# Kernel tuning notes

Hardware: AMD Instinct MI355X
Metric: run time of the kernel (lower is better)

Reference implementation:

```python
import jax, jax.numpy as jnp
import numpy as np

ATTR_LEN = [2, 4, 4, 2, 6]
CUM = np.concatenate(([0], np.cumsum(ATTR_LEN)))  # [0,2,6,10,12,18]
B, S, D, V = 4096, 200, 64, 100000


def setup_inputs() -> dict:
    key = jax.random.key(0)
    ks = jax.random.split(key, 10)
    x = jax.random.randint(ks[0], (B, S), 0, V)
    # one-hot labels per attribute, concatenated -> [B, 18]
    y_parts = []
    for i, al in enumerate(ATTR_LEN):
        lab = jax.random.randint(jax.random.fold_in(ks[1], i), (B,), 0, al)
        y_parts.append(jax.nn.one_hot(lab, al, dtype=jnp.float32))
    y = jnp.concatenate(y_parts, axis=1)
    emb_table = jax.random.normal(ks[2], (V, D), jnp.float32) * 0.02
    emb_table = emb_table.at[0].set(0.0)  # padding_idx=0
    att_w = jax.random.normal(ks[3], (5, D), jnp.float32) * 0.1
    att_b = jax.random.normal(ks[4], (5,), jnp.float32) * 0.1
    W0 = jax.random.normal(ks[5], (ATTR_LEN[0], D), jnp.float32) * 0.1
    W1 = jax.random.normal(ks[6], (ATTR_LEN[1], D), jnp.float32) * 0.1
    W2 = jax.random.normal(ks[7], (ATTR_LEN[2], D), jnp.float32) * 0.1
    W3 = jax.random.normal(ks[8], (ATTR_LEN[3], D), jnp.float32) * 0.1
    W4 = jax.random.normal(ks[9], (ATTR_LEN[4], D), jnp.float32) * 0.1
    return {"x": x, "y": y, "emb_table": emb_table, "att_w": att_w,
            "att_b": att_b, "W0": W0, "W1": W1, "W2": W2, "W3": W3, "W4": W4}


def reference(x, y, emb_table, att_w, att_b, W0, W1, W2, W3, W4):
    embed = emb_table[x]  # [B, S, D] gather (padding row is zero)
    # 5 per-attribute additive tanh-attention heads, batched over k.
    # Softmax over seq axis is independent per head, so stacking is exact.
    att_u = jnp.tanh(jnp.einsum('bsd,kd->bsk', embed, att_w) + att_b)  # [B,S,5]
    score = jax.nn.softmax(att_u, axis=1)                              # [B,S,5]
    user_rep = jnp.einsum('bsd,bsk->bkd', embed, score)                # [B,5,D]
    Ws = [W0, W1, W2, W3, W4]
    # per-task bias-free linear heads, concatenated -> [B, 18]
    W_user = jnp.concatenate([user_rep[:, i] @ Ws[i].T for i in range(5)], axis=1)
    logits = []
    loss = jnp.float32(0.0)
    for i in range(5):
        Wc = W_user[:, CUM[i]:CUM[i + 1]]
        yc = y[:, CUM[i]:CUM[i + 1]]
        # partial_training=False -> ob = ones -> all rows kept;
        # obj = exp(sum(W*y)) / sum_j exp(W_j)  ==  softmax picked at label
        logp = jax.nn.log_softmax(Wc, axis=1)
        loss = loss + (-jnp.sum(logp * yc) / Wc.shape[0])
        logits.append(jax.nn.softmax(Wc, axis=1))
    logit = jnp.concatenate(logits, axis=1)  # [B, 18]
    return logit, loss
```

## Files before the change

kernel.cpp:

```cpp
#include <hip/hip_runtime.h>
#include <math.h>

#define Bsz 4096
#define Ssz 200
#define Dsz 64
#define NK  5
#define NT  512
#define ROWH 72

typedef _Float16 half_t;
typedef _Float16 h2 __attribute__((ext_vector_type(2)));

__device__ inline h2 shfl_xor_h2(h2 v, int m) {
    int iv = __builtin_bit_cast(int, v);
    iv = __shfl_xor(iv, m);
    return __builtin_bit_cast(h2, iv);
}

__device__ inline float fdot2(h2 a, h2 b, float c) {
#if __has_builtin(__builtin_amdgcn_fdot2)
    return __builtin_amdgcn_fdot2(a, b, c, false);
#else
    return c + (float)a.x * (float)b.x + (float)a.y * (float)b.y;
#endif
}

__global__ void loss_reduce_kernel(const float* __restrict__ pb,
                                   float* __restrict__ loss) {
    const int l = threadIdx.x;
    float s = 0.f;
    for (int i = l; i < Bsz; i += 64) s += pb[i];
#pragma unroll
    for (int m = 32; m >= 1; m >>= 1) s += __shfl_xor(s, m);
    if (l == 0) *loss = s * (1.0f / Bsz);
}

__global__ __launch_bounds__(NT, 8) void tan_kernel(
    const int* __restrict__ x, const float* __restrict__ y,
    const float* __restrict__ emb_table,
    const float* __restrict__ att_w, const float* __restrict__ att_b,
    const float* __restrict__ W0, const float* __restrict__ W1,
    const float* __restrict__ W2, const float* __restrict__ W3,
    const float* __restrict__ W4,
    float* __restrict__ out_logit, float* __restrict__ loss_ws)
{
    __shared__ alignas(16) half_t embh[Ssz * ROWH];
    __shared__ alignas(16) float  att[NK][Ssz];
    __shared__ alignas(16) h2     awh[NK * 32];
    __shared__ alignas(16) half_t urph[8][NK][Dsz];
    __shared__ alignas(16) float  ur[NK][Dsz];
    __shared__ alignas(16) int    xs[Ssz];
    __shared__ float wu[18];

    const int b   = blockIdx.x;
    const int tid = threadIdx.x;
    const int w   = tid >> 6;
    const int l   = tid & 63;

    if (tid < Ssz) xs[tid] = x[b * Ssz + tid];
    if (tid >= 256 && tid < 256 + NK * 32) {
        const int t = tid - 256;
        awh[t] = (h2){(half_t)att_w[2 * t], (half_t)att_w[2 * t + 1]};
    }
    __syncthreads();

    {
        float4 v[7];
#pragma unroll
        for (int p = 0; p < 7; ++p) {
            int i = tid + NT * p;
            if (i > Ssz * 16 - 1) i = Ssz * 16 - 1;
            const int s = i >> 4, c = i & 15;
            v[p] = ((const float4*)(emb_table + (size_t)xs[s] * Dsz))[c];
        }
#pragma unroll
        for (int p = 0; p < 7; ++p) {
            const int i = tid + NT * p;
            if (p < 6 || i < Ssz * 16) {
                const int s = i >> 4, c = i & 15;
                h2 a  = (h2){(half_t)v[p].x, (half_t)v[p].y};
                h2 b2 = (h2){(half_t)v[p].z, (half_t)v[p].w};
                uint2 u = { __builtin_bit_cast(unsigned, a),
                            __builtin_bit_cast(unsigned, b2) };
                *(uint2*)(embh + s * ROWH + c * 4) = u;
            }
        }
    }
    __syncthreads();

    if (tid < 2 * Ssz) {
        const int s = tid >> 1, h = tid & 1;
        union { uint4 q[4]; h2 hh[16]; } ue;
        const uint4* rp = (const uint4*)(embh + s * ROWH + h * 32);
#pragma unroll
        for (int i = 0; i < 4; ++i) ue.q[i] = rp[i];
        float acc[NK];
#pragma unroll 1
        for (int k = 0; k < NK; ++k) {
            union { uint4 q[4]; h2 hh[16]; } ua;
            const uint4* ap = (const uint4*)(awh + k * 32 + h * 16);
#pragma unroll
            for (int i = 0; i < 4; ++i) ua.q[i] = ap[i];
            float a = 0.f;
#pragma unroll
            for (int i = 0; i < 16; ++i) a = fdot2(ue.hh[i], ua.hh[i], a);
            acc[k] = a;
        }
#pragma unroll
        for (int k = 0; k < NK; ++k) acc[k] += __shfl_xor(acc[k], 1);
        if (h == 0) {
#pragma unroll
            for (int k = 0; k < NK; ++k) att[k][s] = tanhf(acc[k] + att_b[k]);
        }
    }
    __syncthreads();

    if (w < NK) {
        const int k = w;
        float vals[4];
        float mx = -1e30f;
#pragma unroll
        for (int j = 0; j < 4; ++j) {
            int s = l + 64 * j;
            vals[j] = (s < Ssz) ? att[k][s] : -1e30f;
            mx = fmaxf(mx, vals[j]);
        }
#pragma unroll
        for (int m = 32; m >= 1; m >>= 1) mx = fmaxf(mx, __shfl_xor(mx, m));
        float sum = 0.f;
#pragma unroll
        for (int j = 0; j < 4; ++j) {
            vals[j] = __expf(vals[j] - mx);
            sum += vals[j];
        }
#pragma unroll
        for (int m = 32; m >= 1; m >>= 1) sum += __shfl_xor(sum, m);
        float inv = 1.0f / sum;
#pragma unroll
        for (int j = 0; j < 4; ++j) {
            int s = l + 64 * j;
            if (s < Ssz) att[k][s] = vals[j] * inv;
        }
    }
    __syncthreads();

    {
        const int c = tid & 7;
        const int j = tid >> 3;
        h2 acc[NK][4];
#pragma unroll
        for (int k = 0; k < NK; ++k)
#pragma unroll
            for (int i = 0; i < 4; ++i) acc[k][i] = (h2){(half_t)0, (half_t)0};
#pragma unroll
        for (int t = 0; t < 4; ++t) {
            const int s = j + 64 * t;
            if (s < Ssz) {
                union { uint4 q; h2 hh[4]; } u;
                u.q = *(const uint4*)(embh + s * ROWH + c * 8);
#pragma unroll
                for (int k = 0; k < NK; ++k) {
                    half_t f = (half_t)att[k][s];
                    h2 sc = (h2){f, f};
#pragma unroll
                    for (int i = 0; i < 4; ++i) acc[k][i] += u.hh[i] * sc;
                }
            }
        }
#pragma unroll
        for (int k = 0; k < NK; ++k)
#pragma unroll
            for (int i = 0; i < 4; ++i) {
                acc[k][i] += shfl_xor_h2(acc[k][i], 8);
                acc[k][i] += shfl_xor_h2(acc[k][i], 16);
                acc[k][i] += shfl_xor_h2(acc[k][i], 32);
            }
        if (l < 8) {
#pragma unroll
            for (int k = 0; k < NK; ++k) {
                union { h2 a[4]; uint4 q; } uu;
#pragma unroll
                for (int i = 0; i < 4; ++i) uu.a[i] = acc[k][i];
                *(uint4*)(&urph[w][k][l * 8]) = uu.q;
            }
        }
    }
    __syncthreads();

    if (tid < NK * Dsz) {
        const int k = tid >> 6, d = tid & 63;
        float ssum = 0.f;
#pragma unroll
        for (int jj = 0; jj < 8; ++jj) ssum += (float)urph[jj][k][d];
        ur[k][d] = ssum;
    }
    __syncthreads();

    for (int j = w; j < 18; j += 8) {
        const float* Wp; int g, c0;
        if      (j < 2)  { g = 0; c0 = 0;  Wp = W0; }
        else if (j < 6)  { g = 1; c0 = 2;  Wp = W1; }
        else if (j < 10) { g = 2; c0 = 6;  Wp = W2; }
        else if (j < 12) { g = 3; c0 = 10; Wp = W3; }
        else             { g = 4; c0 = 12; Wp = W4; }
        float p = ur[g][l] * Wp[(j - c0) * Dsz + l];
#pragma unroll
        for (int m = 32; m >= 1; m >>= 1) p += __shfl_xor(p, m);
        if (l == 0) wu[j] = p;
    }
    __syncthreads();

    if (w == 0) {
        float lossb = 0.f;
        if (l < NK) {
            const int LEN[5] = {2, 4, 4, 2, 6};
            const int C0[5]  = {0, 2, 6, 10, 12};
            const int g = l, c0 = C0[g], len = LEN[g];
            float* op = out_logit + (size_t)b * 18;
            const float* yp = y + (size_t)b * 18;
            float mx = -1e30f;
            for (int j = 0; j < len; ++j) mx = fmaxf(mx, wu[c0 + j]);
            float sum = 0.f;
            for (int j = 0; j < len; ++j) sum += __expf(wu[c0 + j] - mx);
            float inv = 1.0f / sum;
            float lse = mx + __logf(sum);
            for (int j = 0; j < len; ++j) {
                op[c0 + j] = __expf(wu[c0 + j] - mx) * inv;
                lossb += (lse - wu[c0 + j]) * yp[c0 + j];
            }
        }
#pragma unroll
        for (int m = 1; m <= 4; m <<= 1) lossb += __shfl_xor(lossb, m);
        if (l == 0) loss_ws[b] = lossb;
    }
}

extern "C" void kernel_launch(void* const* d_in, const int* in_sizes, int n_in,
                              void* d_out, int out_size, void* d_ws, size_t ws_size,
                              hipStream_t stream) {
    const int*   x   = (const int*)d_in[0];
    const float* y   = (const float*)d_in[1];
    const float* emb = (const float*)d_in[2];
    const float* aw  = (const float*)d_in[3];
    const float* ab  = (const float*)d_in[4];
    const float* W0  = (const float*)d_in[5];
    const float* W1  = (const float*)d_in[6];
    const float* W2  = (const float*)d_in[7];
    const float* W3  = (const float*)d_in[8];
    const float* W4  = (const float*)d_in[9];
    float* out  = (float*)d_out;
    float* loss = out + (size_t)Bsz * 18;
    float* pb   = (float*)d_ws;

    tan_kernel<<<Bsz, NT, 0, stream>>>(x, y, emb, aw, ab,
                                       W0, W1, W2, W3, W4, out, pb);
    loss_reduce_kernel<<<1, 64, 0, stream>>>(pb, loss);
}
```

Measured before the change: 164.0 us.

## Compute attention scores with MFMA, store scores in half, atomic loss reduction

Replaces the per-thread fdot2 score computation with 16x16x32 f16 MFMA tiles over padded sequence rows and padded attention weights. Scores are kept in half precision in shared memory, and the weighted-sum stage is re-split to 16 lanes per row. The separate per-head reduction pass and its barrier are folded into the linear-head stage. The final loss is accumulated with a global atomicAdd after a zeroing kernel instead of a second reduction kernel, which changes summation order and adds contention on one address across 4096 blocks.

```diff
diff --git a/kernel.cpp b/kernel.cpp
--- a/kernel.cpp
+++ b/kernel.cpp
@@ -7,9 +7,12 @@
 #define NK  5
 #define NT  512
 #define ROWH 72
+#define AWS  72
 
 typedef _Float16 half_t;
 typedef _Float16 h2 __attribute__((ext_vector_type(2)));
+typedef _Float16 h8 __attribute__((ext_vector_type(8)));
+typedef float    f4v __attribute__((ext_vector_type(4)));
 
 __device__ inline h2 shfl_xor_h2(h2 v, int m) {
     int iv = __builtin_bit_cast(int, v);
@@ -17,22 +20,8 @@
     return __builtin_bit_cast(h2, iv);
 }
 
-__device__ inline float fdot2(h2 a, h2 b, float c) {
-#if __has_builtin(__builtin_amdgcn_fdot2)
-    return __builtin_amdgcn_fdot2(a, b, c, false);
-#else
-    return c + (float)a.x * (float)b.x + (float)a.y * (float)b.y;
-#endif
-}
-
-__global__ void loss_reduce_kernel(const float* __restrict__ pb,
-                                   float* __restrict__ loss) {
-    const int l = threadIdx.x;
-    float s = 0.f;
-    for (int i = l; i < Bsz; i += 64) s += pb[i];
-#pragma unroll
-    for (int m = 32; m >= 1; m >>= 1) s += __shfl_xor(s, m);
-    if (l == 0) *loss = s * (1.0f / Bsz);
+__global__ void zero_loss_kernel(float* loss) {
+    if (threadIdx.x == 0) *loss = 0.0f;
 }
 
 __global__ __launch_bounds__(NT, 8) void tan_kernel(
@@ -42,13 +31,12 @@
     const float* __restrict__ W0, const float* __restrict__ W1,
     const float* __restrict__ W2, const float* __restrict__ W3,
     const float* __restrict__ W4,
-    float* __restrict__ out_logit, float* __restrict__ loss_ws)
+    float* __restrict__ out_logit, float* __restrict__ loss_out)
 {
-    __shared__ alignas(16) half_t embh[Ssz * ROWH];
-    __shared__ alignas(16) float  att[NK][Ssz];
-    __shared__ alignas(16) h2     awh[NK * 32];
+    __shared__ alignas(16) half_t embh[208 * ROWH];
+    __shared__ alignas(16) half_t att_h[NK][208];
+    __shared__ alignas(16) half_t aw_h[16 * AWS];
     __shared__ alignas(16) half_t urph[8][NK][Dsz];
-    __shared__ alignas(16) float  ur[NK][Dsz];
     __shared__ alignas(16) int    xs[Ssz];
     __shared__ float wu[18];
 
@@ -58,9 +46,13 @@
     const int l   = tid & 63;
 
     if (tid < Ssz) xs[tid] = x[b * Ssz + tid];
-    if (tid >= 256 && tid < 256 + NK * 32) {
-        const int t = tid - 256;
-        awh[t] = (h2){(half_t)att_w[2 * t], (half_t)att_w[2 * t + 1]};
+    for (int i = tid; i < 1024; i += NT)
+        aw_h[(i >> 6) * AWS + (i & 63)] =
+            ((i >> 6) < NK) ? (half_t)att_w[i] : (half_t)0;
+    {
+        uint4 zz = {0, 0, 0, 0};
+        uint4* zp = (uint4*)(embh + 200 * ROWH);
+        for (int i = tid; i < 72; i += NT) zp[i] = zz;
     }
     __syncthreads();
 
@@ -88,29 +80,24 @@
     }
     __syncthreads();
 
-    if (tid < 2 * Ssz) {
-        const int s = tid >> 1, h = tid & 1;
-        union { uint4 q[4]; h2 hh[16]; } ue;
-        const uint4* rp = (const uint4*)(embh + s * ROWH + h * 32);
-#pragma unroll
-        for (int i = 0; i < 4; ++i) ue.q[i] = rp[i];
-        float acc[NK];
-#pragma unroll 1
-        for (int k = 0; k < NK; ++k) {
-            union { uint4 q[4]; h2 hh[16]; } ua;
-            const uint4* ap = (const uint4*)(awh + k * 32 + h * 16);
-#pragma unroll
-            for (int i = 0; i < 4; ++i) ua.q[i] = ap[i];
-            float a = 0.f;
-#pragma unroll
-            for (int i = 0; i < 16; ++i) a = fdot2(ue.hh[i], ua.hh[i], a);
-            acc[k] = a;
-        }
-#pragma unroll
-        for (int k = 0; k < NK; ++k) acc[k] += __shfl_xor(acc[k], 1);
-        if (h == 0) {
-#pragma unroll
-            for (int k = 0; k < NK; ++k) att[k][s] = tanhf(acc[k] + att_b[k]);
+    {
+        const int lm = l & 15;
+        const int lq = l >> 4;
+        h8 a0 = *(const h8*)(aw_h + lm * AWS + lq * 8);
+        h8 a1 = *(const h8*)(aw_h + lm * AWS + lq * 8 + 32);
+        for (int t = w; t < 13; t += 8) {
+            const int s = t * 16 + lm;
+            h8 b0 = *(const h8*)(embh + s * ROWH + lq * 8);
+            h8 b1 = *(const h8*)(embh + s * ROWH + lq * 8 + 32);
+            f4v acc = {0.f, 0.f, 0.f, 0.f};
+            acc = __builtin_amdgcn_mfma_f32_16x16x32_f16(a0, b0, acc, 0, 0, 0);
+            acc = __builtin_amdgcn_mfma_f32_16x16x32_f16(a1, b1, acc, 0, 0, 0);
+#pragma unroll
+            for (int r = 0; r < 4; ++r) {
+                const int k = lq * 4 + r;
+                if (k < NK)
+                    att_h[k][s] = (half_t)tanhf(acc[r] + att_b[k]);
+            }
         }
     }
     __syncthreads();
@@ -122,7 +109,7 @@
 #pragma unroll
         for (int j = 0; j < 4; ++j) {
             int s = l + 64 * j;
-            vals[j] = (s < Ssz) ? att[k][s] : -1e30f;
+            vals[j] = (s < Ssz) ? (float)att_h[k][s] : -1e30f;
             mx = fmaxf(mx, vals[j]);
         }
 #pragma unroll
@@ -139,60 +126,49 @@
 #pragma unroll
         for (int j = 0; j < 4; ++j) {
             int s = l + 64 * j;
-            if (s < Ssz) att[k][s] = vals[j] * inv;
-        }
-    }
-    __syncthreads();
-
-    {
-        const int c = tid & 7;
-        const int j = tid >> 3;
-        h2 acc[NK][4];
+            if (s < Ssz) att_h[k][s] = (half_t)(vals[j] * inv);
+        }
+    }
+    __syncthreads();
+
+    {
+        const int c = tid & 15;
+        const int j = tid >> 4;
+        h2 acc[NK][2];
 #pragma unroll
         for (int k = 0; k < NK; ++k)
 #pragma unroll
-            for (int i = 0; i < 4; ++i) acc[k][i] = (h2){(half_t)0, (half_t)0};
-#pragma unroll
-        for (int t = 0; t < 4; ++t) {
-            const int s = j + 64 * t;
+            for (int i = 0; i < 2; ++i) acc[k][i] = (h2){(half_t)0, (half_t)0};
+#pragma unroll
+        for (int t = 0; t < 7; ++t) {
+            const int s = j + 32 * t;
             if (s < Ssz) {
-                union { uint4 q; h2 hh[4]; } u;
-                u.q = *(const uint4*)(embh + s * ROWH + c * 8);
+                union { uint2 q; h2 hh[2]; } u;
+                u.q = *(const uint2*)(embh + s * ROWH + c * 4);
 #pragma unroll
                 for (int k = 0; k < NK; ++k) {
-                    half_t f = (half_t)att[k][s];
+                    half_t f = att_h[k][s];
                     h2 sc = (h2){f, f};
-#pragma unroll
-                    for (int i = 0; i < 4; ++i) acc[k][i] += u.hh[i] * sc;
+                    acc[k][0] += u.hh[0] * sc;
+                    acc[k][1] += u.hh[1] * sc;
                 }
             }
         }
 #pragma unroll
         for (int k = 0; k < NK; ++k)
 #pragma unroll
-            for (int i = 0; i < 4; ++i) {
-                acc[k][i] += shfl_xor_h2(acc[k][i], 8);
+            for (int i = 0; i < 2; ++i) {
                 acc[k][i] += shfl_xor_h2(acc[k][i], 16);
                 acc[k][i] += shfl_xor_h2(acc[k][i], 32);
             }
-        if (l < 8) {
+        if (l < 16) {
 #pragma unroll
             for (int k = 0; k < NK; ++k) {
-                union { h2 a[4]; uint4 q; } uu;
-#pragma unroll
-                for (int i = 0; i < 4; ++i) uu.a[i] = acc[k][i];
-                *(uint4*)(&urph[w][k][l * 8]) = uu.q;
-            }
-        }
-    }
-    __syncthreads();
-
-    if (tid < NK * Dsz) {
-        const int k = tid >> 6, d = tid & 63;
-        float ssum = 0.f;
-#pragma unroll
-        for (int jj = 0; jj < 8; ++jj) ssum += (float)urph[jj][k][d];
-        ur[k][d] = ssum;
+                union { h2 a[2]; uint2 q; } uu;
+                uu.a[0] = acc[k][0]; uu.a[1] = acc[k][1];
+                *(uint2*)(&urph[w][k][l * 4]) = uu.q;
+            }
+        }
     }
     __syncthreads();
 
@@ -203,7 +179,10 @@
         else if (j < 10) { g = 2; c0 = 6;  Wp = W2; }
         else if (j < 12) { g = 3; c0 = 10; Wp = W3; }
         else             { g = 4; c0 = 12; Wp = W4; }
-        float p = ur[g][l] * Wp[(j - c0) * Dsz + l];
+        float urv = 0.f;
+#pragma unroll
+        for (int jj = 0; jj < 8; ++jj) urv += (float)urph[jj][g][l];
+        float p = urv * Wp[(j - c0) * Dsz + l];
 #pragma unroll
         for (int m = 32; m >= 1; m >>= 1) p += __shfl_xor(p, m);
         if (l == 0) wu[j] = p;
@@ -231,7 +210,7 @@
         }
 #pragma unroll
         for (int m = 1; m <= 4; m <<= 1) lossb += __shfl_xor(lossb, m);
-        if (l == 0) loss_ws[b] = lossb;
+        if (l == 0) atomicAdd(loss_out, lossb * (1.0f / Bsz));
     }
 }
 
@@ -250,9 +229,8 @@
     const float* W4  = (const float*)d_in[9];
     float* out  = (float*)d_out;
     float* loss = out + (size_t)Bsz * 18;
-    float* pb   = (float*)d_ws;
-
+
+    zero_loss_kernel<<<1, 64, 0, stream>>>(loss);
     tan_kernel<<<Bsz, NT, 0, stream>>>(x, y, emb, aw, ab,
-                                       W0, W1, W2, W3, W4, out, pb);
-    loss_reduce_kernel<<<1, 64, 0, stream>>>(pb, loss);
-}
+                                       W0, W1, W2, W3, W4, out, loss);
+}
```

New measurement: 156.8 us. -4.4%, faster.
